# Optimization experiments

Measured on AMD Instinct MI355X. Metric: run time of the kernel, lower is better.

Reference implementation:

```python
import jax, jax.numpy as jnp
import numpy as np

N_NODES = 100000
N_EDGES = 1600000
HIDDEN = 128
IN_FEAT = 7
N_CLASSES = 2
N_GRAPHS = 512


def _glorot(key, shape):
    lim = float(np.sqrt(6.0 / (shape[0] + shape[1])))
    return jax.random.uniform(key, shape, jnp.float32, -lim, lim)


def setup_inputs() -> dict:
    key = jax.random.key(0)
    ks = jax.random.split(key, 8)
    x = jax.random.normal(ks[0], (N_NODES, IN_FEAT), jnp.float32)
    edge_index = jax.random.randint(ks[1], (2, N_EDGES), 0, N_NODES, jnp.int32)
    batch_data = jnp.sort(jax.random.randint(ks[2], (N_NODES,), 0, N_GRAPHS, jnp.int32))
    return {
        "x": x,
        "edge_index": edge_index,
        "batch_data": batch_data,
        "W1": _glorot(ks[3], (IN_FEAT, HIDDEN)),
        "b1": jnp.zeros((HIDDEN,), jnp.float32),
        "W2": _glorot(ks[4], (HIDDEN, HIDDEN)),
        "b2": jnp.zeros((HIDDEN,), jnp.float32),
        "W3": _glorot(ks[5], (HIDDEN, HIDDEN)),
        "b3": jnp.zeros((HIDDEN,), jnp.float32),
        "Wl": _glorot(ks[6], (HIDDEN, N_CLASSES)),
        "bl": jnp.zeros((N_CLASSES,), jnp.float32),
    }


def reference(x, edge_index, batch_data, W1, b1, W2, b2, W3, b3, Wl, bl):
    n = x.shape[0]
    loops = jnp.arange(n, dtype=edge_index.dtype)
    src = jnp.concatenate([edge_index[0], loops])  # [E+N]
    dst = jnp.concatenate([edge_index[1], loops])
    # GCN symmetric normalization with self-loops (PyG gcn_norm default)
    deg = jax.ops.segment_sum(jnp.ones_like(dst, dtype=x.dtype), dst, num_segments=n)
    dis = jax.lax.rsqrt(deg)  # deg >= 1 thanks to self-loops
    norm = (dis[src] * dis[dst])[:, None]  # [E+N, 1]

    def gcn_relu(h, W, b):
        hw = h @ W                                  # [N, H] linear first (PyG GCNConv)
        msg = hw[src] * norm                        # gather + edge-normalize
        agg = jax.ops.segment_sum(msg, dst, num_segments=n)  # scatter-add
        return jax.nn.relu(agg + b)

    h = gcn_relu(x, W1, b1)
    h = gcn_relu(h, W2, b2)
    h = gcn_relu(h, W3, b3)
    pooled = jax.ops.segment_max(h, batch_data, num_segments=N_GRAPHS)  # [G, H]
    return pooled @ Wl + bl
```

## Files before the change

### kernel.cpp

```cpp
#include <hip/hip_runtime.h>
#include <hip/hip_fp16.h>

#define N_NODES 100000
#define N_EDGES 1600000
#define HID 128
#define N_GRAPHS 512
#define NBK 196
#define SEG 8192

typedef _Float16 f16x8 __attribute__((ext_vector_type(8)));
typedef float f32x4 __attribute__((ext_vector_type(4)));


__global__ void k_bhist(const int* __restrict__ dst, int e, int* __restrict__ bkcnt) {
    __shared__ int l[NBK];
    int tid = threadIdx.x;
    for (int i = tid; i < NBK; i += 256) l[i] = 0;
    __syncthreads();
    int base = blockIdx.x * SEG;
    int m = min(SEG, e - base);
    for (int i = tid; i < m; i += 256) atomicAdd(&l[dst[base + i] >> 9], 1);
    __syncthreads();
    for (int b = tid; b < NBK; b += 256)
        if (l[b]) atomicAdd(&bkcnt[b], l[b]);
}

__global__ void k_bscan(const int* __restrict__ bkcnt, int* __restrict__ bkoff,
                        int* __restrict__ bcur, int e) {
    __shared__ int s[256];
    int t = threadIdx.x;
    int v = (t < NBK) ? bkcnt[t] : 0;
    s[t] = v;
    __syncthreads();
    for (int off = 1; off < 256; off <<= 1) {
        int u = (t >= off) ? s[t - off] : 0;
        __syncthreads();
        s[t] += u;
        __syncthreads();
    }
    int excl = s[t] - v;
    if (t < NBK) { bkoff[t] = excl; bcur[t] = excl; }
    if (t == NBK - 1) bkoff[NBK] = excl + v;
}

__launch_bounds__(256) __global__
void k_passA(const int* __restrict__ ei, int* __restrict__ bcur,
             unsigned* __restrict__ pk, int e) {
    __shared__ int lcnt[NBK];
    __shared__ int lbase[NBK];
    int tid = threadIdx.x;
    int base = blockIdx.x * SEG;
    for (int i = tid; i < NBK; i += 256) lcnt[i] = 0;
    __syncthreads();
    int m = min(SEG, e - base);
    for (int i = tid; i < m; i += 256) {
        int d = ei[N_EDGES + base + i];
        atomicAdd(&lcnt[d >> 9], 1);
    }
    __syncthreads();
    for (int b = tid; b < NBK; b += 256)
        lbase[b] = lcnt[b] ? atomicAdd(&bcur[b], lcnt[b]) : 0;
    __syncthreads();
    for (int i = tid; i < m; i += 256) {
        int s = ei[base + i];
        int d = ei[N_EDGES + base + i];
        int pos = atomicAdd(&lbase[d >> 9], 1);
        pk[pos] = ((unsigned)s << 9) | (unsigned)(d & 511);
    }
}

__launch_bounds__(256) __global__
void k_passB(const unsigned* __restrict__ pk, const int* __restrict__ bkoff,
             int* __restrict__ rowptr, float* __restrict__ dis, float* __restrict__ dinv,
             int* __restrict__ csrc, int n, int e) {
    __shared__ int lcnt[512];
    __shared__ int lofs[512];
    __shared__ int sw[256];
    int b = blockIdx.x;
    int tid = threadIdx.x;
    int db0 = b * 512;
    int nd = min(512, n - db0);
    int pbeg = bkoff[b];
    int pend = bkoff[b + 1];
    lcnt[tid] = 0;
    lcnt[tid + 256] = 0;
    __syncthreads();
    for (int i = pbeg + tid; i < pend; i += 256) atomicAdd(&lcnt[pk[i] & 511], 1);
    __syncthreads();
    for (int j = tid; j < nd; j += 256) {
        float d = (float)(lcnt[j] + 1);
        dis[db0 + j] = rsqrtf(d);
        dinv[db0 + j] = 1.0f / d;
    }
    int a0 = lcnt[2 * tid];
    int a1 = lcnt[2 * tid + 1];
    int v = a0 + a1;
    sw[tid] = v;
    __syncthreads();
    for (int off = 1; off < 256; off <<= 1) {
        int u = (tid >= off) ? sw[tid - off] : 0;
        __syncthreads();
        sw[tid] += u;
        __syncthreads();
    }
    int excl = sw[tid] - v;
    lofs[2 * tid] = excl;
    lofs[2 * tid + 1] = excl + a0;
    __syncthreads();
    for (int j = tid; j < nd; j += 256) rowptr[db0 + j] = pbeg + lofs[j];
    if (db0 + nd == n && tid == 0) rowptr[n] = e;
    for (int j = tid; j < 512; j += 256) lcnt[j] = pbeg + lofs[j];
    __syncthreads();
    for (int i = pbeg + tid; i < pend; i += 256) {
        unsigned w = pk[i];
        int pos = atomicAdd(&lcnt[w & 511], 1);
        csrc[pos] = (int)(w >> 9);
    }
}


__global__ void k_padx(const float* __restrict__ x, float* __restrict__ x8, int n) {
    int i = blockIdx.x * 256 + threadIdx.x;
    if (i >= n * 8) return;
    int node = i >> 3;
    int k = i & 7;
    x8[i] = (k < 7) ? x[node * 7 + k] : 0.f;
}


__launch_bounds__(256) __global__
void k_gather7(const int* __restrict__ rowptr, const int* __restrict__ csrc,
               const float* __restrict__ dis, const float* __restrict__ dinv,
               const float2* __restrict__ x8v, float2* __restrict__ aggxv, int n) {
    int idx = blockIdx.x * 256 + threadIdx.x;
    int node = idx >> 2;
    if (node >= n) return;
    int qq = idx & 3;
    int beg = rowptr[node];
    int end = rowptr[node + 1];
    float dd = dis[node];
    float di = dinv[node];
    float2 acc = make_float2(0.f, 0.f);
    int j = beg;
    for (; j + 1 < end; j += 2) {
        int s0 = csrc[j];
        int s1 = csrc[j + 1];
        float w0 = dis[s0];
        float w1 = dis[s1];
        float2 v0 = x8v[(size_t)s0 * 4 + qq];
        float2 v1 = x8v[(size_t)s1 * 4 + qq];
        acc.x += v0.x * w0 + v1.x * w1;
        acc.y += v0.y * w0 + v1.y * w1;
    }
    if (j < end) {
        int s0 = csrc[j];
        float w0 = dis[s0];
        float2 v0 = x8v[(size_t)s0 * 4 + qq];
        acc.x += v0.x * w0;
        acc.y += v0.y * w0;
    }
    float2 ps = x8v[(size_t)node * 4 + qq];
    float2 r;
    r.x = ps.x * di + dd * acc.x;
    r.y = ps.y * di + dd * acc.y;
    aggxv[(size_t)node * 4 + qq] = r;
}


__device__ __forceinline__ int swz(int row, int kByte) {
    return row * 256 + (kByte ^ ((row & 7) << 4));
}

__launch_bounds__(256) __global__
void k_l12(const float2* __restrict__ aggxv, const float* __restrict__ b1,
           const float* __restrict__ W1, const float* __restrict__ W2,
           __half* __restrict__ hwout, int n) {
    __shared__ __align__(16) _Float16 Wt[128 * 128];
    __shared__ __align__(16) _Float16 As[64 * 128];
    int tid = threadIdx.x;

    for (int i = tid; i < 128 * 128; i += 256) {
        int k = i >> 7;
        int nn = i & 127;
        *(_Float16*)((char*)Wt + swz(nn, k * 2)) = (_Float16)W2[i];
    }

    int rg = tid >> 5;
    int c4 = tid & 31;
    int col = c4 * 4;
    float4 w1k[7];
#pragma unroll
    for (int k = 0; k < 7; ++k) w1k[k] = *(const float4*)(W1 + k * 128 + col);
    float4 bb = *(const float4*)(b1 + col);

    int wv = tid >> 6;
    int lane = tid & 63;
    int lo16 = lane & 15;
    int hi4 = lane >> 4;

    for (int t = 0; t < 2; ++t) {
        if (t) __syncthreads();
#pragma unroll
        for (int rl = 0; rl < 8; ++rl) {
            int row = rg * 8 + rl;
            int grow = blockIdx.x * 128 + t * 64 + row;
            uint2 pk2 = make_uint2(0u, 0u);
            if (grow < n) {
                float2 a0 = aggxv[(size_t)grow * 4 + 0];
                float2 a1 = aggxv[(size_t)grow * 4 + 1];
                float2 a2 = aggxv[(size_t)grow * 4 + 2];
                float2 a3 = aggxv[(size_t)grow * 4 + 3];
                float4 acc = bb;
                acc.x += a0.x*w1k[0].x + a0.y*w1k[1].x + a1.x*w1k[2].x + a1.y*w1k[3].x
                       + a2.x*w1k[4].x + a2.y*w1k[5].x + a3.x*w1k[6].x;
                acc.y += a0.x*w1k[0].y + a0.y*w1k[1].y + a1.x*w1k[2].y + a1.y*w1k[3].y
                       + a2.x*w1k[4].y + a2.y*w1k[5].y + a3.x*w1k[6].y;
                acc.z += a0.x*w1k[0].z + a0.y*w1k[1].z + a1.x*w1k[2].z + a1.y*w1k[3].z
                       + a2.x*w1k[4].z + a2.y*w1k[5].z + a3.x*w1k[6].z;
                acc.w += a0.x*w1k[0].w + a0.y*w1k[1].w + a1.x*w1k[2].w + a1.y*w1k[3].w
                       + a2.x*w1k[4].w + a2.y*w1k[5].w + a3.x*w1k[6].w;
                __half2 h0 = __floats2half2_rn(fmaxf(acc.x, 0.f), fmaxf(acc.y, 0.f));
                __half2 h1 = __floats2half2_rn(fmaxf(acc.z, 0.f), fmaxf(acc.w, 0.f));
                pk2.x = *(unsigned*)&h0;
                pk2.y = *(unsigned*)&h1;
            }
            *(uint2*)((char*)As + swz(row, c4 * 8)) = pk2;
        }
        __syncthreads();

        f32x4 acc[8];
#pragma unroll
        for (int nt = 0; nt < 8; ++nt) acc[nt] = (f32x4){0.f, 0.f, 0.f, 0.f};
        const char* Ab = (const char*)As;
        const char* Bb = (const char*)Wt;
#pragma unroll
        for (int kt = 0; kt < 4; ++kt) {
            int kByte = kt * 64 + hi4 * 16;
            f16x8 af = *(const f16x8*)(Ab + swz(wv * 16 + lo16, kByte));
#pragma unroll
            for (int nt = 0; nt < 8; ++nt) {
                f16x8 bf = *(const f16x8*)(Bb + swz(nt * 16 + lo16, kByte));
                acc[nt] = __builtin_amdgcn_mfma_f32_16x16x32_f16(af, bf, acc[nt], 0, 0, 0);
            }
        }
        int rbase = blockIdx.x * 128 + t * 64 + wv * 16 + hi4 * 4;
#pragma unroll
        for (int nt = 0; nt < 8; ++nt) {
#pragma unroll
            for (int r = 0; r < 4; ++r) {
                int node = rbase + r;
                if (node < n)
                    hwout[(size_t)node * 128 + nt * 16 + lo16] = __float2half_rn(acc[nt][r]);
            }
        }
    }
}


__device__ __forceinline__ void acc8(uint2 p, float w, float4& a) {
    float2 lo = __half22float2(*(__half2*)&p.x);
    float2 hi = __half22float2(*(__half2*)&p.y);
    a.x += lo.x * w; a.y += lo.y * w; a.z += hi.x * w; a.w += hi.y * w;
}

__launch_bounds__(256) __global__
void k_gather(const int* __restrict__ rowptr, const int* __restrict__ csrc,
              const float* __restrict__ dis, const float* __restrict__ dinv,
              const uint2* __restrict__ hwv, uint2* __restrict__ aggv, int n) {
    int wid = blockIdx.x * 4 + (threadIdx.x >> 6);
    int lane = threadIdx.x & 63;
    int sub = lane >> 5;
    int c = lane & 31;
    int node = wid * 2 + sub;
    if (node >= n) return;

    int beg = rowptr[node];
    int end = rowptr[node + 1];
    int deg = end - beg;
    float dd = dis[node];
    float di = dinv[node];

    int sidx = 0;
    float wsc = 0.f;
    if (c < deg) {
        sidx = csrc[beg + c];
        wsc = dis[sidx];
    }

    int mown = deg < 32 ? deg : 32;
    int m = max(__shfl(mown, 0), __shfl(mown, 32));
    int sub32 = sub << 5;

    float4 a = make_float4(0.f, 0.f, 0.f, 0.f);
    int j = 0;
    for (; j + 7 < m; j += 8) {
        int s0 = __shfl(sidx, sub32 + j);     float w0 = __shfl(wsc, sub32 + j);
        int s1 = __shfl(sidx, sub32 + j + 1); float w1 = __shfl(wsc, sub32 + j + 1);
        int s2 = __shfl(sidx, sub32 + j + 2); float w2 = __shfl(wsc, sub32 + j + 2);
        int s3 = __shfl(sidx, sub32 + j + 3); float w3 = __shfl(wsc, sub32 + j + 3);
        int s4 = __shfl(sidx, sub32 + j + 4); float w4 = __shfl(wsc, sub32 + j + 4);
        int s5 = __shfl(sidx, sub32 + j + 5); float w5 = __shfl(wsc, sub32 + j + 5);
        int s6 = __shfl(sidx, sub32 + j + 6); float w6 = __shfl(wsc, sub32 + j + 6);
        int s7 = __shfl(sidx, sub32 + j + 7); float w7 = __shfl(wsc, sub32 + j + 7);
        uint2 p0 = hwv[(size_t)s0 * 32 + c];
        uint2 p1 = hwv[(size_t)s1 * 32 + c];
        uint2 p2 = hwv[(size_t)s2 * 32 + c];
        uint2 p3 = hwv[(size_t)s3 * 32 + c];
        uint2 p4 = hwv[(size_t)s4 * 32 + c];
        uint2 p5 = hwv[(size_t)s5 * 32 + c];
        uint2 p6 = hwv[(size_t)s6 * 32 + c];
        uint2 p7 = hwv[(size_t)s7 * 32 + c];
        acc8(p0, w0, a); acc8(p1, w1, a); acc8(p2, w2, a); acc8(p3, w3, a);
        acc8(p4, w4, a); acc8(p5, w5, a); acc8(p6, w6, a); acc8(p7, w7, a);
    }
    for (; j < m; ++j) {
        int s0 = __shfl(sidx, sub32 + j);
        float w0 = __shfl(wsc, sub32 + j);
        uint2 p0 = hwv[(size_t)s0 * 32 + c];
        acc8(p0, w0, a);
    }
    for (int jj = beg + 32; jj < end; ++jj) {
        int s0 = csrc[jj];
        float w0 = dis[s0];
        uint2 p0 = hwv[(size_t)s0 * 32 + c];
        acc8(p0, w0, a);
    }

    uint2 ps = hwv[(size_t)node * 32 + c];
    float2 slo = __half22float2(*(__half2*)&ps.x);
    float2 shi = __half22float2(*(__half2*)&ps.y);
    float4 r;
    r.x = slo.x * di + dd * a.x;
    r.y = slo.y * di + dd * a.y;
    r.z = shi.x * di + dd * a.z;
    r.w = shi.y * di + dd * a.w;
    __half2 lo = __floats2half2_rn(r.x, r.y);
    __half2 hi = __floats2half2_rn(r.z, r.w);
    uint2 o;
    o.x = *(unsigned*)&lo;
    o.y = *(unsigned*)&hi;
    aggv[(size_t)node * 32 + c] = o;
}


__launch_bounds__(256) __global__
void k_gemm_mfma(const __half* __restrict__ aggin, const float* __restrict__ b,
                 const float* __restrict__ W, __half* __restrict__ hwout, int n) {
    __shared__ __align__(16) _Float16 Wt[128 * 128];
    __shared__ __align__(16) _Float16 As[64 * 128];
    int tid = threadIdx.x;

    for (int i = tid; i < 128 * 128; i += 256) {
        int k = i >> 7;
        int nn = i & 127;
        *(_Float16*)((char*)Wt + swz(nn, k * 2)) = (_Float16)W[i];
    }

    int row = tid >> 2;
    int q = tid & 3;
    int wv = tid >> 6;
    int lane = tid & 63;
    int lo16 = lane & 15;
    int hi4 = lane >> 4;

    for (int t = 0; t < 2; ++t) {
        if (t) __syncthreads();
        int grow = blockIdx.x * 128 + t * 64 + row;
#pragma unroll
        for (int j = 0; j < 4; ++j) {
            int c0 = q * 32 + j * 8;
            uint4 pk = make_uint4(0u, 0u, 0u, 0u);
            if (grow < n) {
                uint4 p = *(const uint4*)(aggin + (size_t)grow * 128 + c0);
                float4 bA = *(const float4*)(b + c0);
                float4 bB = *(const float4*)(b + c0 + 4);
                float2 t0 = __half22float2(*(const __half2*)&p.x);
                float2 t1 = __half22float2(*(const __half2*)&p.y);
                float2 t2 = __half22float2(*(const __half2*)&p.z);
                float2 t3 = __half22float2(*(const __half2*)&p.w);
                __half2 h0 = __floats2half2_rn(fmaxf(t0.x + bA.x, 0.f), fmaxf(t0.y + bA.y, 0.f));
                __half2 h1 = __floats2half2_rn(fmaxf(t1.x + bA.z, 0.f), fmaxf(t1.y + bA.w, 0.f));
                __half2 h2 = __floats2half2_rn(fmaxf(t2.x + bB.x, 0.f), fmaxf(t2.y + bB.y, 0.f));
                __half2 h3 = __floats2half2_rn(fmaxf(t3.x + bB.z, 0.f), fmaxf(t3.y + bB.w, 0.f));
                pk.x = *(unsigned*)&h0; pk.y = *(unsigned*)&h1;
                pk.z = *(unsigned*)&h2; pk.w = *(unsigned*)&h3;
            }
            *(uint4*)((char*)As + swz(row, c0 * 2)) = pk;
        }
        __syncthreads();

        f32x4 acc[8];
#pragma unroll
        for (int nt = 0; nt < 8; ++nt) acc[nt] = (f32x4){0.f, 0.f, 0.f, 0.f};

        const char* Ab = (const char*)As;
        const char* Bb = (const char*)Wt;
#pragma unroll
        for (int kt = 0; kt < 4; ++kt) {
            int kByte = kt * 64 + hi4 * 16;
            f16x8 af = *(const f16x8*)(Ab + swz(wv * 16 + lo16, kByte));
#pragma unroll
            for (int nt = 0; nt < 8; ++nt) {
                f16x8 bf = *(const f16x8*)(Bb + swz(nt * 16 + lo16, kByte));
                acc[nt] = __builtin_amdgcn_mfma_f32_16x16x32_f16(af, bf, acc[nt], 0, 0, 0);
            }
        }

        int rbase = blockIdx.x * 128 + t * 64 + wv * 16 + hi4 * 4;
#pragma unroll
        for (int nt = 0; nt < 8; ++nt) {
#pragma unroll
            for (int r = 0; r < 4; ++r) {
                int node = rbase + r;
                if (node < n)
                    hwout[(size_t)node * 128 + nt * 16 + lo16] = __float2half_rn(acc[nt][r]);
            }
        }
    }
}


__global__ void k_pool_max(const __half* __restrict__ agg, const float* __restrict__ b,
                           const int* __restrict__ batch, unsigned* __restrict__ pooled, int n) {
    int idx = blockIdx.x * 256 + threadIdx.x;
    int node = idx >> 7;
    if (node >= n) return;
    int c = idx & 127;
    int g = batch[node];
    float v = __half2float(agg[(size_t)node * 128 + c]) + b[c];
    v = fmaxf(v, 0.f);
    atomicMax(&pooled[(size_t)g * 128 + c], __float_as_uint(v));
}


__global__ void k_final(const float* __restrict__ pooled, const float* __restrict__ Wl,
                        const float* __restrict__ bl, float* __restrict__ out) {
    int g = blockIdx.x;
    int t = threadIdx.x;
    float p0 = pooled[(size_t)g * 128 + t];
    float p1 = pooled[(size_t)g * 128 + t + 64];
    float a0 = p0 * Wl[t * 2 + 0] + p1 * Wl[(t + 64) * 2 + 0];
    float a1 = p0 * Wl[t * 2 + 1] + p1 * Wl[(t + 64) * 2 + 1];
#pragma unroll
    for (int off = 32; off > 0; off >>= 1) {
        a0 += __shfl_down(a0, off);
        a1 += __shfl_down(a1, off);
    }
    if (t == 0) {
        out[g * 2 + 0] = a0 + bl[0];
        out[g * 2 + 1] = a1 + bl[1];
    }
}


extern "C" void kernel_launch(void* const* d_in, const int* in_sizes, int n_in,
                              void* d_out, int out_size, void* d_ws, size_t ws_size,
                              hipStream_t stream) {
    const float* x  = (const float*)d_in[0];
    const int*   ei = (const int*)d_in[1];
    const int*   batch = (const int*)d_in[2];
    const float* W1 = (const float*)d_in[3];
    const float* b1 = (const float*)d_in[4];
    const float* W2 = (const float*)d_in[5];
    const float* b2 = (const float*)d_in[6];
    const float* W3 = (const float*)d_in[7];
    const float* b3 = (const float*)d_in[8];
    const float* Wl = (const float*)d_in[9];
    const float* bl = (const float*)d_in[10];
    float* out = (float*)d_out;

    const int N = N_NODES, E = N_EDGES;

    char* ws = (char*)d_ws;
    __half* bufA = (__half*)ws;
    __half* bufB = bufA + (size_t)N * 128;
    unsigned* pooled = (unsigned*)(bufB + (size_t)N * 128);
    float* dis  = (float*)(pooled + (size_t)N_GRAPHS * 128);
    float* dinv = dis + N;
    int*   rowptr = (int*)(dinv + N);
    int*   bkcnt  = rowptr + N + 2;
    int*   bkoff  = bkcnt + 256;
    int*   bcur   = bkoff + 256;
    int*   csrc   = bcur + 256;
    unsigned* pk  = (unsigned*)(csrc + E);
    float* x8   = (float*)pk;
    float* aggx = x8 + (size_t)N * 8;

    hipMemsetAsync(bkcnt, 0, NBK * sizeof(int), stream);
    int nseg = (E + SEG - 1) / SEG;
    k_bhist<<<nseg, 256, 0, stream>>>(ei + E, E, bkcnt);
    k_bscan<<<1, 256, 0, stream>>>(bkcnt, bkoff, bcur, E);
    k_passA<<<nseg, 256, 0, stream>>>(ei, bcur, pk, E);
    k_passB<<<NBK, 256, 0, stream>>>(pk, bkoff, rowptr, dis, dinv, csrc, N, E);

    int ggrid = (N + 7) / 8;
    int mfma_grid = (N + 127) / 128;

    k_padx<<<(N * 8 + 255) / 256, 256, 0, stream>>>(x, x8, N);
    k_gather7<<<(N * 4 + 255) / 256, 256, 0, stream>>>(rowptr, csrc, dis, dinv,
                                                       (const float2*)x8, (float2*)aggx, N);
    k_l12<<<mfma_grid, 256, 0, stream>>>((const float2*)aggx, b1, W1, W2, bufA, N);

    k_gather<<<ggrid, 256, 0, stream>>>(rowptr, csrc, dis, dinv,
                                        (const uint2*)bufA, (uint2*)bufB, N);
    k_gemm_mfma<<<mfma_grid, 256, 0, stream>>>(bufB, b2, W3, bufA, N);

    k_gather<<<ggrid, 256, 0, stream>>>(rowptr, csrc, dis, dinv,
                                        (const uint2*)bufA, (uint2*)bufB, N);
    hipMemsetAsync(pooled, 0, (size_t)N_GRAPHS * 128 * sizeof(unsigned), stream);
    k_pool_max<<<(N * 128 + 255) / 256, 256, 0, stream>>>(bufB, b3, batch, pooled, N);

    k_final<<<N_GRAPHS, 64, 0, stream>>>((const float*)pooled, Wl, bl, out);
}
```

Before: 391.2 us.

## Widen gather loads, pre-convert weights to fp16, shrink CSR buckets, enlarge GEMM tiles

The gather kernel now has 16 lanes per node, each loading uint4 (8 halves), with neighbour indices held in two shuffle registers, instead of 32 lanes loading uint2. A small kernel converts W2 and W3 to transposed fp16 once, so the GEMM blocks stage weights with vector copies instead of per-element float-to-half conversion. The CSR build uses 256-node buckets with smaller segments, which gives more blocks in passB. GEMM blocks now process 256 rows each, so the weight staging cost is spread over more rows at the price of fewer blocks.

```diff
diff --git a/kernel.cpp b/kernel.cpp
--- a/kernel.cpp
+++ b/kernel.cpp
@@ -5,8 +5,8 @@
 #define N_EDGES 1600000
 #define HID 128
 #define N_GRAPHS 512
-#define NBK 196
-#define SEG 8192
+#define NBK 391
+#define SEG 4096
 
 typedef _Float16 f16x8 __attribute__((ext_vector_type(8)));
 typedef float f32x4 __attribute__((ext_vector_type(4)));
@@ -19,7 +19,7 @@
     __syncthreads();
     int base = blockIdx.x * SEG;
     int m = min(SEG, e - base);
-    for (int i = tid; i < m; i += 256) atomicAdd(&l[dst[base + i] >> 9], 1);
+    for (int i = tid; i < m; i += 256) atomicAdd(&l[dst[base + i] >> 8], 1);
     __syncthreads();
     for (int b = tid; b < NBK; b += 256)
         if (l[b]) atomicAdd(&bkcnt[b], l[b]);
@@ -27,12 +27,12 @@
 
 __global__ void k_bscan(const int* __restrict__ bkcnt, int* __restrict__ bkoff,
                         int* __restrict__ bcur, int e) {
-    __shared__ int s[256];
+    __shared__ int s[512];
     int t = threadIdx.x;
     int v = (t < NBK) ? bkcnt[t] : 0;
     s[t] = v;
     __syncthreads();
-    for (int off = 1; off < 256; off <<= 1) {
+    for (int off = 1; off < 512; off <<= 1) {
         int u = (t >= off) ? s[t - off] : 0;
         __syncthreads();
         s[t] += u;
@@ -55,7 +55,7 @@
     int m = min(SEG, e - base);
     for (int i = tid; i < m; i += 256) {
         int d = ei[N_EDGES + base + i];
-        atomicAdd(&lcnt[d >> 9], 1);
+        atomicAdd(&lcnt[d >> 8], 1);
     }
     __syncthreads();
     for (int b = tid; b < NBK; b += 256)
@@ -64,8 +64,8 @@
     for (int i = tid; i < m; i += 256) {
         int s = ei[base + i];
         int d = ei[N_EDGES + base + i];
-        int pos = atomicAdd(&lbase[d >> 9], 1);
-        pk[pos] = ((unsigned)s << 9) | (unsigned)(d & 511);
+        int pos = atomicAdd(&lbase[d >> 8], 1);
+        pk[pos] = ((unsigned)s << 8) | (unsigned)(d & 255);
     }
 }
 
@@ -73,28 +73,24 @@
 void k_passB(const unsigned* __restrict__ pk, const int* __restrict__ bkoff,
              int* __restrict__ rowptr, float* __restrict__ dis, float* __restrict__ dinv,
              int* __restrict__ csrc, int n, int e) {
-    __shared__ int lcnt[512];
-    __shared__ int lofs[512];
+    __shared__ int lcnt[256];
     __shared__ int sw[256];
     int b = blockIdx.x;
     int tid = threadIdx.x;
-    int db0 = b * 512;
-    int nd = min(512, n - db0);
+    int db0 = b * 256;
+    int nd = min(256, n - db0);
     int pbeg = bkoff[b];
     int pend = bkoff[b + 1];
     lcnt[tid] = 0;
-    lcnt[tid + 256] = 0;
-    __syncthreads();
-    for (int i = pbeg + tid; i < pend; i += 256) atomicAdd(&lcnt[pk[i] & 511], 1);
-    __syncthreads();
-    for (int j = tid; j < nd; j += 256) {
-        float d = (float)(lcnt[j] + 1);
-        dis[db0 + j] = rsqrtf(d);
-        dinv[db0 + j] = 1.0f / d;
-    }
-    int a0 = lcnt[2 * tid];
-    int a1 = lcnt[2 * tid + 1];
-    int v = a0 + a1;
+    __syncthreads();
+    for (int i = pbeg + tid; i < pend; i += 256) atomicAdd(&lcnt[pk[i] & 255], 1);
+    __syncthreads();
+    if (tid < nd) {
+        float d = (float)(lcnt[tid] + 1);
+        dis[db0 + tid] = rsqrtf(d);
+        dinv[db0 + tid] = 1.0f / d;
+    }
+    int v = lcnt[tid];
     sw[tid] = v;
     __syncthreads();
     for (int off = 1; off < 256; off <<= 1) {
@@ -104,18 +100,26 @@
         __syncthreads();
     }
     int excl = sw[tid] - v;
-    lofs[2 * tid] = excl;
-    lofs[2 * tid + 1] = excl + a0;
-    __syncthreads();
-    for (int j = tid; j < nd; j += 256) rowptr[db0 + j] = pbeg + lofs[j];
+    if (tid < nd) rowptr[db0 + tid] = pbeg + excl;
     if (db0 + nd == n && tid == 0) rowptr[n] = e;
-    for (int j = tid; j < 512; j += 256) lcnt[j] = pbeg + lofs[j];
+    lcnt[tid] = pbeg + excl;
     __syncthreads();
     for (int i = pbeg + tid; i < pend; i += 256) {
         unsigned w = pk[i];
-        int pos = atomicAdd(&lcnt[w & 511], 1);
-        csrc[pos] = (int)(w >> 9);
-    }
+        int pos = atomicAdd(&lcnt[w & 255], 1);
+        csrc[pos] = (int)(w >> 8);
+    }
+}
+
+
+__global__ void k_prepW(const float* __restrict__ W2, const float* __restrict__ W3,
+                        __half* __restrict__ w2h, __half* __restrict__ w3h) {
+    int i = blockIdx.x * 256 + threadIdx.x;
+    if (i >= 128 * 128) return;
+    int nn = i >> 7;
+    int k = i & 127;
+    w2h[i] = __float2half_rn(W2[k * 128 + nn]);
+    w3h[i] = __float2half_rn(W3[k * 128 + nn]);
 }
 
 
@@ -167,23 +171,128 @@
 }
 
 
+__device__ __forceinline__ void acc16(uint4 p, float w, float4& lo, float4& hi) {
+    float2 t0 = __half22float2(*(__half2*)&p.x);
+    float2 t1 = __half22float2(*(__half2*)&p.y);
+    float2 t2 = __half22float2(*(__half2*)&p.z);
+    float2 t3 = __half22float2(*(__half2*)&p.w);
+    lo.x += t0.x * w; lo.y += t0.y * w; lo.z += t1.x * w; lo.w += t1.y * w;
+    hi.x += t2.x * w; hi.y += t2.y * w; hi.z += t3.x * w; hi.w += t3.y * w;
+}
+
+__launch_bounds__(256) __global__
+void k_gather(const int* __restrict__ rowptr, const int* __restrict__ csrc,
+              const float* __restrict__ dis, const float* __restrict__ dinv,
+              const uint4* __restrict__ hwv, uint4* __restrict__ aggv, int n) {
+    int wid = blockIdx.x * 4 + (threadIdx.x >> 6);
+    int lane = threadIdx.x & 63;
+    int grp = lane >> 4;
+    int c = lane & 15;
+    int node = wid * 4 + grp;
+    if (node >= n) return;
+
+    int beg = rowptr[node];
+    int end = rowptr[node + 1];
+    int deg = end - beg;
+    float dd = dis[node];
+    float di = dinv[node];
+
+    int s0i = 0, s1i = 0;
+    float w0r = 0.f, w1r = 0.f;
+    if (c < deg)      { s0i = csrc[beg + c];      w0r = dis[s0i]; }
+    if (c + 16 < deg) { s1i = csrc[beg + 16 + c]; w1r = dis[s1i]; }
+
+    int m = deg < 32 ? deg : 32;
+    m = max(m, __shfl_xor(m, 16));
+    m = max(m, __shfl_xor(m, 32));
+    int g16 = grp << 4;
+
+    float4 alo = make_float4(0.f, 0.f, 0.f, 0.f);
+    float4 ahi = make_float4(0.f, 0.f, 0.f, 0.f);
+
+    int m0 = m < 16 ? m : 16;
+    int j = 0;
+    for (; j + 3 < m0; j += 4) {
+        int a0 = __shfl(s0i, g16 + j);     float b0 = __shfl(w0r, g16 + j);
+        int a1 = __shfl(s0i, g16 + j + 1); float b1 = __shfl(w0r, g16 + j + 1);
+        int a2 = __shfl(s0i, g16 + j + 2); float b2 = __shfl(w0r, g16 + j + 2);
+        int a3 = __shfl(s0i, g16 + j + 3); float b3 = __shfl(w0r, g16 + j + 3);
+        uint4 p0 = hwv[(size_t)a0 * 16 + c];
+        uint4 p1 = hwv[(size_t)a1 * 16 + c];
+        uint4 p2 = hwv[(size_t)a2 * 16 + c];
+        uint4 p3 = hwv[(size_t)a3 * 16 + c];
+        acc16(p0, b0, alo, ahi); acc16(p1, b1, alo, ahi);
+        acc16(p2, b2, alo, ahi); acc16(p3, b3, alo, ahi);
+    }
+    for (; j < m0; ++j) {
+        int a0 = __shfl(s0i, g16 + j);
+        float b0 = __shfl(w0r, g16 + j);
+        uint4 p0 = hwv[(size_t)a0 * 16 + c];
+        acc16(p0, b0, alo, ahi);
+    }
+    int j2 = 16;
+    for (; j2 + 3 < m; j2 += 4) {
+        int a0 = __shfl(s1i, g16 + j2 - 16); float b0 = __shfl(w1r, g16 + j2 - 16);
+        int a1 = __shfl(s1i, g16 + j2 - 15); float b1 = __shfl(w1r, g16 + j2 - 15);
+        int a2 = __shfl(s1i, g16 + j2 - 14); float b2 = __shfl(w1r, g16 + j2 - 14);
+        int a3 = __shfl(s1i, g16 + j2 - 13); float b3 = __shfl(w1r, g16 + j2 - 13);
+        uint4 p0 = hwv[(size_t)a0 * 16 + c];
+        uint4 p1 = hwv[(size_t)a1 * 16 + c];
+        uint4 p2 = hwv[(size_t)a2 * 16 + c];
+        uint4 p3 = hwv[(size_t)a3 * 16 + c];
+        acc16(p0, b0, alo, ahi); acc16(p1, b1, alo, ahi);
+        acc16(p2, b2, alo, ahi); acc16(p3, b3, alo, ahi);
+    }
+    for (; j2 < m; ++j2) {
+        int a0 = __shfl(s1i, g16 + j2 - 16);
+        float b0 = __shfl(w1r, g16 + j2 - 16);
+        uint4 p0 = hwv[(size_t)a0 * 16 + c];
+        acc16(p0, b0, alo, ahi);
+    }
+    for (int jj = beg + 32; jj < end; ++jj) {
+        int s = csrc[jj];
+        float w = dis[s];
+        uint4 p = hwv[(size_t)s * 16 + c];
+        acc16(p, w, alo, ahi);
+    }
+
+    uint4 ps = hwv[(size_t)node * 16 + c];
+    float2 q0 = __half22float2(*(__half2*)&ps.x);
+    float2 q1 = __half22float2(*(__half2*)&ps.y);
+    float2 q2 = __half22float2(*(__half2*)&ps.z);
+    float2 q3 = __half22float2(*(__half2*)&ps.w);
+    __half2 h0 = __floats2half2_rn(q0.x * di + dd * alo.x, q0.y * di + dd * alo.y);
+    __half2 h1 = __floats2half2_rn(q1.x * di + dd * alo.z, q1.y * di + dd * alo.w);
+    __half2 h2 = __floats2half2_rn(q2.x * di + dd * ahi.x, q2.y * di + dd * ahi.y);
+    __half2 h3 = __floats2half2_rn(q3.x * di + dd * ahi.z, q3.y * di + dd * ahi.w);
+    uint4 o;
+    o.x = *(unsigned*)&h0; o.y = *(unsigned*)&h1;
+    o.z = *(unsigned*)&h2; o.w = *(unsigned*)&h3;
+    aggv[(size_t)node * 16 + c] = o;
+}
+
+
 __device__ __forceinline__ int swz(int row, int kByte) {
     return row * 256 + (kByte ^ ((row & 7) << 4));
 }
 
+__device__ __forceinline__ void stageW(const __half* __restrict__ wh, _Float16* Wt, int tid) {
+    for (int i = tid; i < 128 * 16; i += 256) {
+        int nn = i >> 4;
+        int kq = i & 15;
+        uint4 v = ((const uint4*)wh)[i];
+        *(uint4*)((char*)Wt + swz(nn, kq * 16)) = v;
+    }
+}
+
 __launch_bounds__(256) __global__
 void k_l12(const float2* __restrict__ aggxv, const float* __restrict__ b1,
-           const float* __restrict__ W1, const float* __restrict__ W2,
+           const float* __restrict__ W1, const __half* __restrict__ w2h,
            __half* __restrict__ hwout, int n) {
     __shared__ __align__(16) _Float16 Wt[128 * 128];
     __shared__ __align__(16) _Float16 As[64 * 128];
     int tid = threadIdx.x;
-
-    for (int i = tid; i < 128 * 128; i += 256) {
-        int k = i >> 7;
-        int nn = i & 127;
-        *(_Float16*)((char*)Wt + swz(nn, k * 2)) = (_Float16)W2[i];
-    }
+    stageW(w2h, Wt, tid);
 
     int rg = tid >> 5;
     int c4 = tid & 31;
@@ -198,12 +307,12 @@
     int lo16 = lane & 15;
     int hi4 = lane >> 4;
 
-    for (int t = 0; t < 2; ++t) {
+    for (int t = 0; t < 4; ++t) {
         if (t) __syncthreads();
 #pragma unroll
         for (int rl = 0; rl < 8; ++rl) {
             int row = rg * 8 + rl;
-            int grow = blockIdx.x * 128 + t * 64 + row;
+            int grow = blockIdx.x * 256 + t * 64 + row;
             uint2 pk2 = make_uint2(0u, 0u);
             if (grow < n) {
                 float2 a0 = aggxv[(size_t)grow * 4 + 0];
@@ -243,7 +352,7 @@
                 acc[nt] = __builtin_amdgcn_mfma_f32_16x16x32_f16(af, bf, acc[nt], 0, 0, 0);
             }
         }
-        int rbase = blockIdx.x * 128 + t * 64 + wv * 16 + hi4 * 4;
+        int rbase = blockIdx.x * 256 + t * 64 + wv * 16 + hi4 * 4;
 #pragma unroll
         for (int nt = 0; nt < 8; ++nt) {
 #pragma unroll
@@ -257,104 +366,13 @@
 }
 
 
-__device__ __forceinline__ void acc8(uint2 p, float w, float4& a) {
-    float2 lo = __half22float2(*(__half2*)&p.x);
-    float2 hi = __half22float2(*(__half2*)&p.y);
-    a.x += lo.x * w; a.y += lo.y * w; a.z += hi.x * w; a.w += hi.y * w;
-}
-
-__launch_bounds__(256) __global__
-void k_gather(const int* __restrict__ rowptr, const int* __restrict__ csrc,
-              const float* __restrict__ dis, const float* __restrict__ dinv,
-              const uint2* __restrict__ hwv, uint2* __restrict__ aggv, int n) {
-    int wid = blockIdx.x * 4 + (threadIdx.x >> 6);
-    int lane = threadIdx.x & 63;
-    int sub = lane >> 5;
-    int c = lane & 31;
-    int node = wid * 2 + sub;
-    if (node >= n) return;
-
-    int beg = rowptr[node];
-    int end = rowptr[node + 1];
-    int deg = end - beg;
-    float dd = dis[node];
-    float di = dinv[node];
-
-    int sidx = 0;
-    float wsc = 0.f;
-    if (c < deg) {
-        sidx = csrc[beg + c];
-        wsc = dis[sidx];
-    }
-
-    int mown = deg < 32 ? deg : 32;
-    int m = max(__shfl(mown, 0), __shfl(mown, 32));
-    int sub32 = sub << 5;
-
-    float4 a = make_float4(0.f, 0.f, 0.f, 0.f);
-    int j = 0;
-    for (; j + 7 < m; j += 8) {
-        int s0 = __shfl(sidx, sub32 + j);     float w0 = __shfl(wsc, sub32 + j);
-        int s1 = __shfl(sidx, sub32 + j + 1); float w1 = __shfl(wsc, sub32 + j + 1);
-        int s2 = __shfl(sidx, sub32 + j + 2); float w2 = __shfl(wsc, sub32 + j + 2);
-        int s3 = __shfl(sidx, sub32 + j + 3); float w3 = __shfl(wsc, sub32 + j + 3);
-        int s4 = __shfl(sidx, sub32 + j + 4); float w4 = __shfl(wsc, sub32 + j + 4);
-        int s5 = __shfl(sidx, sub32 + j + 5); float w5 = __shfl(wsc, sub32 + j + 5);
-        int s6 = __shfl(sidx, sub32 + j + 6); float w6 = __shfl(wsc, sub32 + j + 6);
-        int s7 = __shfl(sidx, sub32 + j + 7); float w7 = __shfl(wsc, sub32 + j + 7);
-        uint2 p0 = hwv[(size_t)s0 * 32 + c];
-        uint2 p1 = hwv[(size_t)s1 * 32 + c];
-        uint2 p2 = hwv[(size_t)s2 * 32 + c];
-        uint2 p3 = hwv[(size_t)s3 * 32 + c];
-        uint2 p4 = hwv[(size_t)s4 * 32 + c];
-        uint2 p5 = hwv[(size_t)s5 * 32 + c];
-        uint2 p6 = hwv[(size_t)s6 * 32 + c];
-        uint2 p7 = hwv[(size_t)s7 * 32 + c];
-        acc8(p0, w0, a); acc8(p1, w1, a); acc8(p2, w2, a); acc8(p3, w3, a);
-        acc8(p4, w4, a); acc8(p5, w5, a); acc8(p6, w6, a); acc8(p7, w7, a);
-    }
-    for (; j < m; ++j) {
-        int s0 = __shfl(sidx, sub32 + j);
-        float w0 = __shfl(wsc, sub32 + j);
-        uint2 p0 = hwv[(size_t)s0 * 32 + c];
-        acc8(p0, w0, a);
-    }
-    for (int jj = beg + 32; jj < end; ++jj) {
-        int s0 = csrc[jj];
-        float w0 = dis[s0];
-        uint2 p0 = hwv[(size_t)s0 * 32 + c];
-        acc8(p0, w0, a);
-    }
-
-    uint2 ps = hwv[(size_t)node * 32 + c];
-    float2 slo = __half22float2(*(__half2*)&ps.x);
-    float2 shi = __half22float2(*(__half2*)&ps.y);
-    float4 r;
-    r.x = slo.x * di + dd * a.x;
-    r.y = slo.y * di + dd * a.y;
-    r.z = shi.x * di + dd * a.z;
-    r.w = shi.y * di + dd * a.w;
-    __half2 lo = __floats2half2_rn(r.x, r.y);
-    __half2 hi = __floats2half2_rn(r.z, r.w);
-    uint2 o;
-    o.x = *(unsigned*)&lo;
-    o.y = *(unsigned*)&hi;
-    aggv[(size_t)node * 32 + c] = o;
-}
-
-
 __launch_bounds__(256) __global__
 void k_gemm_mfma(const __half* __restrict__ aggin, const float* __restrict__ b,
-                 const float* __restrict__ W, __half* __restrict__ hwout, int n) {
+                 const __half* __restrict__ wh, __half* __restrict__ hwout, int n) {
     __shared__ __align__(16) _Float16 Wt[128 * 128];
     __shared__ __align__(16) _Float16 As[64 * 128];
     int tid = threadIdx.x;
-
-    for (int i = tid; i < 128 * 128; i += 256) {
-        int k = i >> 7;
-        int nn = i & 127;
-        *(_Float16*)((char*)Wt + swz(nn, k * 2)) = (_Float16)W[i];
-    }
+    stageW(wh, Wt, tid);
 
     int row = tid >> 2;
     int q = tid & 3;
@@ -363,9 +381,9 @@
     int lo16 = lane & 15;
     int hi4 = lane >> 4;
 
-    for (int t = 0; t < 2; ++t) {
+    for (int t = 0; t < 4; ++t) {
         if (t) __syncthreads();
-        int grow = blockIdx.x * 128 + t * 64 + row;
+        int grow = blockIdx.x * 256 + t * 64 + row;
 #pragma unroll
         for (int j = 0; j < 4; ++j) {
             int c0 = q * 32 + j * 8;
@@ -406,7 +424,7 @@
             }
         }
 
-        int rbase = blockIdx.x * 128 + t * 64 + wv * 16 + hi4 * 4;
+        int rbase = blockIdx.x * 256 + t * 64 + wv * 16 + hi4 * 4;
 #pragma unroll
         for (int nt = 0; nt < 8; ++nt) {
 #pragma unroll
@@ -479,34 +497,38 @@
     float* dinv = dis + N;
     int*   rowptr = (int*)(dinv + N);
     int*   bkcnt  = rowptr + N + 2;
-    int*   bkoff  = bkcnt + 256;
-    int*   bcur   = bkoff + 256;
-    int*   csrc   = bcur + 256;
+    int*   bkoff  = bkcnt + 512;
+    int*   bcur   = bkoff + 512;
+    int*   csrc   = bcur + 512;
     unsigned* pk  = (unsigned*)(csrc + E);
     float* x8   = (float*)pk;
     float* aggx = x8 + (size_t)N * 8;
+    __half* w2h = (__half*)(pk + E);
+    __half* w3h = w2h + 128 * 128;
 
     hipMemsetAsync(bkcnt, 0, NBK * sizeof(int), stream);
     int nseg = (E + SEG - 1) / SEG;
     k_bhist<<<nseg, 256, 0, stream>>>(ei + E, E, bkcnt);
-    k_bscan<<<1, 256, 0, stream>>>(bkcnt, bkoff, bcur, E);
+    k_bscan<<<1, 512, 0, stream>>>(bkcnt, bkoff, bcur, E);
     k_passA<<<nseg, 256, 0, stream>>>(ei, bcur, pk, E);
     k_passB<<<NBK, 256, 0, stream>>>(pk, bkoff, rowptr, dis, dinv, csrc, N, E);
 
-    int ggrid = (N + 7) / 8;
-    int mfma_grid = (N + 127) / 128;
+    k_prepW<<<64, 256, 0, stream>>>(W2, W3, w2h, w3h);
+
+    int ggrid = (N + 15) / 16;
+    int mfma_grid = (N + 255) / 256;
 
     k_padx<<<(N * 8 + 255) / 256, 256, 0, stream>>>(x, x8, N);
     k_gather7<<<(N * 4 + 255) / 256, 256, 0, stream>>>(rowptr, csrc, dis, dinv,
                                                        (const float2*)x8, (float2*)aggx, N);
-    k_l12<<<mfma_grid, 256, 0, stream>>>((const float2*)aggx, b1, W1, W2, bufA, N);
+    k_l12<<<mfma_grid, 256, 0, stream>>>((const float2*)aggx, b1, W1, w2h, bufA, N);
 
     k_gather<<<ggrid, 256, 0, stream>>>(rowptr, csrc, dis, dinv,
-                                        (const uint2*)bufA, (uint2*)bufB, N);
-    k_gemm_mfma<<<mfma_grid, 256, 0, stream>>>(bufB, b2, W3, bufA, N);
+                                        (const uint4*)bufA, (uint4*)bufB, N);
+    k_gemm_mfma<<<mfma_grid, 256, 0, stream>>>(bufB, b2, w3h, bufA, N);
 
     k_gather<<<ggrid, 256, 0, stream>>>(rowptr, csrc, dis, dinv,
-                                        (const uint2*)bufA, (uint2*)bufB, N);
+                                        (const uint4*)bufA, (uint4*)bufB, N);
     hipMemsetAsync(pooled, 0, (size_t)N_GRAPHS * 128 * sizeof(unsigned), stream);
     k_pool_max<<<(N * 128 + 255) / 256, 256, 0, stream>>>(bufB, b3, batch, pooled, N);
 
```

New measurement: 389.9 us. Within noise of the previous version (-0.3%).
